# Kernel tuning notes

Hardware: AMD Instinct MI355X
Metric: run time of the kernel (lower is better)

Reference implementation:

```python
import jax, jax.numpy as jnp
import numpy as np


def _mask_finished_scores(score, flag):
    # score: (B, K); flag: (B, 1) bool. For finished rows: column 0 -> 0, columns > 0 -> -inf
    # (standard WeNet mask_finished_scores, applied both to (B, beam) and (B, V) tensors).
    K = score.shape[-1]
    col = jnp.arange(K)[None, :]
    score = jnp.where(flag & (col == 0), 0.0, score)
    return jnp.where(flag & (col > 0), -jnp.inf, score)


def _batch_beam_search(log_post, beam_size, masks):
    # log_post: (B, S, V) log-softmax; masks: (B, S) bool (True = padded/finished)
    B, S, V = log_post.shape
    eos = V - 1
    log_prob, idx0 = jax.lax.top_k(log_post[:, 0, :], beam_size)   # (B, beam)
    end_flag = masks[:, 0][:, None]                                # (B, 1)
    log_prob = _mask_finished_scores(log_prob, end_flag)
    idx0 = jnp.where(end_flag, eos, idx0)                          # mask_finished_preds

    def step(carry, xs):
        log_prob, end_flag = carry
        lp_i, m_i = xs                                             # (B, V), (B,)
        scores = _mask_finished_scores(lp_i, end_flag)             # (B, V)
        cand = log_prob[:, :, None] + scores[:, None, :]           # (B, beam, V)
        log_prob, top_idx = jax.lax.top_k(cand.reshape(B, beam_size * V), beam_size)
        idx = jnp.where(end_flag, eos, top_idx)                    # mask_finished_preds
        return (log_prob, m_i[:, None]), idx

    (log_prob, _), idx_rest = jax.lax.scan(
        step,
        (log_prob, end_flag),
        (jnp.swapaxes(log_post[:, 1:], 0, 1), jnp.swapaxes(masks[:, 1:], 0, 1)),
    )
    indices = jnp.concatenate([idx0[None], idx_rest], axis=0)      # (S, B, beam)
    indices = jnp.moveaxis(indices, 0, -1)                         # (B, beam, S)
    return jnp.mod(indices, V), log_prob                           # torch.fmod(indices, vocab)


def setup_inputs() -> dict:
    key = jax.random.key(0)
    k1, k2, k3 = jax.random.split(key, 3)
    B, S, V, BEAM = 16, 128, 32000, 4
    logit = jax.random.normal(k1, (B, S, V), dtype=jnp.float32)
    asd_scores = jax.random.uniform(k2, (BEAM, B), dtype=jnp.float32)
    tgt_lens = jax.random.randint(k3, (B,), 0, S)
    return {"logit": logit, "asd_scores": asd_scores, "tgt_lens": tgt_lens, "beam_size": BEAM}


def reference(logit, asd_scores, tgt_lens, beam_size):
    B, S, V = logit.shape
    lens = jnp.clip(tgt_lens, 2, S)
    # make_pad_mask(tgt_lens - 1): True where position is padding
    masks = jnp.arange(S)[None, :] >= (lens - 1)[:, None]          # (B, S) bool
    log_post = jax.nn.log_softmax(logit, axis=-1)                  # (B, S, V)
    # beam search runs under no_grad in torch -> stop_gradient here
    indices, _ = _batch_beam_search(jax.lax.stop_gradient(log_post), beam_size, masks)
    # gather per-step log-probs along each beam path: (B, beam, S)
    glp = jnp.take_along_axis(log_post[:, None], indices[..., None], axis=-1).squeeze(-1)
    topk_log_prob = jnp.sum(jnp.where(masks[:, None, :], 0.0, glp), axis=-1)  # (B, beam)
    nbest_log_dist = topk_log_prob.T                               # (beam, B)
    # compute_masd_loss_ver2 with normalized_score=True
    w = jax.nn.softmax(nbest_log_dist, axis=0)                     # exp(d - logsumexp(d, 0))
    asd_norm = asd_scores - jnp.mean(asd_scores, axis=0)           # (beam, B)
    masd = jnp.sum(w * asd_norm, axis=0)                           # (B,)
    return jnp.mean(masd)                                          # reduction='mean'
```

## Files before the change

### kernel.cpp

```cpp
#include <hip/hip_runtime.h>
#include <math.h>

#define NB 16
#define NS 128
#define NV 32000
#define ROWS (NB*NS)
#define CAP 1024
#define T0  3.0f

#define WS_IX_OFF  (ROWS*4*sizeof(float))
#define WS_PART_OFF (WS_IX_OFF + ROWS*4*sizeof(unsigned short))

__device__ __forceinline__ bool lexgt(float av, int ai, float bv, int bi) {
    return (av > bv) || (av == bv && ai < bi);
}

__global__ __launch_bounds__(256)
void k_rowprep(const float* __restrict__ logit,
               float* __restrict__ ws_sc,
               unsigned short* __restrict__ ws_ix)
{
    const int row  = blockIdx.x;
    const int tid  = threadIdx.x;
    const int lane = tid & 63;
    const int wv   = tid >> 6;
    const float4* __restrict__ x4 = (const float4*)(logit + (size_t)row * NV);

    __shared__ float  sM[4];
    __shared__ double sE[4];
    __shared__ int    s_cnt;
    __shared__ __align__(16) char smem[16384];
    float* s_cv = (float*)smem;
    int*   s_ci = (int*)(smem + CAP*4);
    float* stv  = (float*)smem;
    int*   sti  = (int*)(smem + 8192);

    if (tid == 0) s_cnt = 0;
    __syncthreads();

    float m = -INFINITY;
    double e0 = 0.0, e1 = 0.0, e2 = 0.0, e3 = 0.0;

#define PROC(q, base)                                                                            \
    {                                                                                            \
        float mx = fmaxf(fmaxf((q).x, (q).y), fmaxf((q).z, (q).w));                              \
        m = fmaxf(m, mx);                                                                        \
        e0 += (double)__expf((q).x);                                                             \
        e1 += (double)__expf((q).y);                                                             \
        e2 += (double)__expf((q).z);                                                             \
        e3 += (double)__expf((q).w);                                                             \
        if (mx >= T0) {                                                                          \
            if ((q).x >= T0) { int p = atomicAdd(&s_cnt, 1); if (p < CAP) { s_cv[p] = (q).x; s_ci[p] = 4*(base)+0; } } \
            if ((q).y >= T0) { int p = atomicAdd(&s_cnt, 1); if (p < CAP) { s_cv[p] = (q).y; s_ci[p] = 4*(base)+1; } } \
            if ((q).z >= T0) { int p = atomicAdd(&s_cnt, 1); if (p < CAP) { s_cv[p] = (q).z; s_ci[p] = 4*(base)+2; } } \
            if ((q).w >= T0) { int p = atomicAdd(&s_cnt, 1); if (p < CAP) { s_cv[p] = (q).w; s_ci[p] = 4*(base)+3; } } \
        }                                                                                        \
    }

#pragma unroll 1
    for (int k = 0; k < 7; ++k) {
        const int i = tid + k*1024;
        float4 q0 = x4[i];
        float4 q1 = x4[i + 256];
        float4 q2 = x4[i + 512];
        float4 q3 = x4[i + 768];
        PROC(q0, i);
        PROC(q1, i + 256);
        PROC(q2, i + 512);
        PROC(q3, i + 768);
    }
    for (int i = 7168 + tid; i < NV/4; i += 256) {
        float4 q = x4[i];
        PROC(q, i);
    }
#undef PROC

    float gm = m;
    gm = fmaxf(gm, __shfl_xor(gm, 1));
    gm = fmaxf(gm, __shfl_xor(gm, 2));
    gm = fmaxf(gm, __shfl_xor(gm, 4));
    float Tw = gm;
    Tw = fminf(Tw, __shfl_xor(Tw, 8));
    Tw = fminf(Tw, __shfl_xor(Tw, 16));
    Tw = fminf(Tw, __shfl_xor(Tw, 32));
    float wm = gm;
    wm = fmaxf(wm, __shfl_xor(wm, 8));
    wm = fmaxf(wm, __shfl_xor(wm, 16));
    wm = fmaxf(wm, __shfl_xor(wm, 32));
    double es = ((e0 + e1) + (e2 + e3));
    es += __shfl_xor(es, 1);
    es += __shfl_xor(es, 2);
    es += __shfl_xor(es, 4);
    es += __shfl_xor(es, 8);
    es += __shfl_xor(es, 16);
    es += __shfl_xor(es, 32);

    if (lane == 0) { sM[wv] = wm; sE[wv] = es; }
    __syncthreads();

    const float  M    = fmaxf(fmaxf(sM[0], sM[1]), fmaxf(sM[2], sM[3]));
    const double Esum = ((sE[0] + sE[1]) + (sE[2] + sE[3]));
    int cnt = s_cnt;

    bool fast = (cnt >= 8) && (cnt <= CAP);
    if (!fast) {
        __syncthreads();
        if (tid == 0) s_cnt = 0;
        __syncthreads();
        for (int i = tid; i < NV/4; i += 256) {
            float4 q = x4[i];
            float mx = fmaxf(fmaxf(q.x, q.y), fmaxf(q.z, q.w));
            if (mx >= Tw) {
                if (q.x >= Tw) { int p = atomicAdd(&s_cnt, 1); if (p < CAP) { s_cv[p] = q.x; s_ci[p] = 4*i+0; } }
                if (q.y >= Tw) { int p = atomicAdd(&s_cnt, 1); if (p < CAP) { s_cv[p] = q.y; s_ci[p] = 4*i+1; } }
                if (q.z >= Tw) { int p = atomicAdd(&s_cnt, 1); if (p < CAP) { s_cv[p] = q.z; s_ci[p] = 4*i+2; } }
                if (q.w >= Tw) { int p = atomicAdd(&s_cnt, 1); if (p < CAP) { s_cv[p] = q.w; s_ci[p] = 4*i+3; } }
            }
        }
        __syncthreads();
        cnt = s_cnt;
    }

    if (cnt <= CAP) {
        if (wv == 0) {
            float tv[8]; int ti[8];
#pragma unroll
            for (int j = 0; j < 8; ++j) { tv[j] = -INFINITY; ti[j] = 0x7fffffff; }
            for (int c = lane; c < cnt; c += 64) {
                float v = s_cv[c]; int gi = s_ci[c];
                if (lexgt(v, gi, tv[7], ti[7])) {
                    tv[7] = v; ti[7] = gi;
#pragma unroll
                    for (int p = 7; p > 0; --p) {
                        if (lexgt(tv[p], ti[p], tv[p-1], ti[p-1])) {
                            float fv = tv[p]; tv[p] = tv[p-1]; tv[p-1] = fv;
                            int   fi = ti[p]; ti[p] = ti[p-1]; ti[p-1] = fi;
                        }
                    }
                }
            }
            float bv[8]; int bi[8];
#pragma unroll
            for (int r = 0; r < 8; ++r) {
                float hv = tv[0]; int hi = ti[0];
#pragma unroll
                for (int d = 1; d <= 32; d <<= 1) {
                    float ov = __shfl_xor(hv, d); int oi = __shfl_xor(hi, d);
                    if (lexgt(ov, oi, hv, hi)) { hv = ov; hi = oi; }
                }
                bv[r] = hv; bi[r] = hi;
                if (ti[0] == hi) {
#pragma unroll
                    for (int p = 0; p < 7; ++p) { tv[p] = tv[p+1]; ti[p] = ti[p+1]; }
                    tv[7] = -INFINITY; ti[7] = 0x7fffffff;
                }
            }
            if (lane == 0) {
                float slse = (float)(log(Esum) - (double)M);
                float sc[8]; int ix[8];
#pragma unroll
                for (int j = 0; j < 8; ++j) { sc[j] = (bv[j] - M) - slse; ix[j] = bi[j]; }
#pragma unroll
                for (int pass = 0; pass < 8; ++pass) {
#pragma unroll
                    for (int j = 0; j < 7; ++j) {
                        if (lexgt(sc[j+1], ix[j+1], sc[j], ix[j])) {
                            float fv = sc[j]; sc[j] = sc[j+1]; sc[j+1] = fv;
                            int   fi = ix[j]; ix[j] = ix[j+1]; ix[j+1] = fi;
                        }
                    }
                }
#pragma unroll
                for (int j = 0; j < 4; ++j) {
                    ws_sc[row*4+j] = sc[j];
                    ws_ix[row*4+j] = (unsigned short)ix[j];
                }
            }
        }
    } else {
        float tv[8]; int ti[8];
#pragma unroll
        for (int j = 0; j < 8; ++j) { tv[j] = -INFINITY; ti[j] = 0x7fffffff; }
        for (int i = tid; i < NV/4; i += 256) {
            float4 q = x4[i];
#pragma unroll
            for (int c = 0; c < 4; ++c) {
                float v = (c==0)?q.x:(c==1)?q.y:(c==2)?q.z:q.w;
                int gi = 4*i + c;
                if (lexgt(v, gi, tv[7], ti[7])) {
                    tv[7] = v; ti[7] = gi;
#pragma unroll
                    for (int p = 7; p > 0; --p) {
                        if (lexgt(tv[p], ti[p], tv[p-1], ti[p-1])) {
                            float fv = tv[p]; tv[p] = tv[p-1]; tv[p-1] = fv;
                            int   fi = ti[p]; ti[p] = ti[p-1]; ti[p-1] = fi;
                        }
                    }
                }
            }
        }
        __syncthreads();
#pragma unroll
        for (int j = 0; j < 8; ++j) { stv[tid*8+j] = tv[j]; sti[tid*8+j] = ti[j]; }
        __syncthreads();
        for (int st = 128; st >= 1; st >>= 1) {
            if (tid < st) {
                int pa = 0, pb = 0;
                float ov[8]; int oi[8];
#pragma unroll
                for (int j = 0; j < 8; ++j) {
                    float av = stv[tid*8+pa];      int aix = sti[tid*8+pa];
                    float bv = stv[(tid+st)*8+pb]; int bix = sti[(tid+st)*8+pb];
                    bool ta = lexgt(av, aix, bv, bix);
                    ov[j] = ta ? av : bv;
                    oi[j] = ta ? aix : bix;
                    pa += ta ? 1 : 0;
                    pb += ta ? 0 : 1;
                }
#pragma unroll
                for (int j = 0; j < 8; ++j) { stv[tid*8+j] = ov[j]; sti[tid*8+j] = oi[j]; }
            }
            __syncthreads();
        }
        if (tid == 0) {
            float slse = (float)(log(Esum) - (double)M);
            float sc[8]; int ix[8];
#pragma unroll
            for (int j = 0; j < 8; ++j) { sc[j] = (stv[j] - M) - slse; ix[j] = sti[j]; }
#pragma unroll
            for (int pass = 0; pass < 8; ++pass) {
#pragma unroll
                for (int j = 0; j < 7; ++j) {
                    if (lexgt(sc[j+1], ix[j+1], sc[j], ix[j])) {
                        float fv = sc[j]; sc[j] = sc[j+1]; sc[j+1] = fv;
                        int   fi = ix[j]; ix[j] = ix[j+1]; ix[j+1] = fi;
                    }
                }
            }
#pragma unroll
            for (int j = 0; j < 4; ++j) {
                ws_sc[row*4+j] = sc[j];
                ws_ix[row*4+j] = (unsigned short)ix[j];
            }
        }
    }
}

__global__ __launch_bounds__(64)
void k_beam(const float* __restrict__ ws_sc,
            const unsigned short* __restrict__ ws_ix,
            const float* __restrict__ asd,
            const int*   __restrict__ tlen,
            float* __restrict__ ws_part)
{
    const int b = blockIdx.x;
    const int lane = threadIdx.x;

    __shared__ float4  Lsc[NS];
    __shared__ ushort4 Lix[NS];
    {
        const float4*  sc4p = (const float4*)ws_sc;
        const ushort4* ix4p = (const ushort4*)ws_ix;
        for (int i = lane; i < NS; i += 64) {
            Lsc[i] = sc4p[b*NS + i];
            Lix[i] = ix4p[b*NS + i];
        }
    }
    __syncthreads();

    int L = tlen[b];
    L = L < 2 ? 2 : (L > NS ? NS : L);

    const int ci = lane & 15;
    const int k  = ci >> 2;
    const int r  = ci & 3;

    float4 sc0 = Lsc[0];
    float c0 = sc0.x, c1 = sc0.y, c2 = sc0.z, c3 = sc0.w;
    double sum0 = sc0.x, sum1 = sc0.y, sum2 = sc0.z, sum3 = sc0.w;

    float4 scN = Lsc[1]; ushort4 ixN = Lix[1];

    for (int s = 1; s <= L-2; ++s) {
        float4 sc = scN; ushort4 ix = ixN;
        scN = Lsc[s+1]; ixN = Lix[s+1];

        float myscore = (r==0)?sc.x:(r==1)?sc.y:(r==2)?sc.z:sc.w;
        int   myidx   = (r==0)?ix.x:(r==1)?ix.y:(r==2)?ix.z:ix.w;
        float mycarry = (k==0)?c0:(k==1)?c1:(k==2)?c2:c3;
        float cand = mycarry + myscore;
        int   flat = k*NV + myidx;

        int g = lane >> 4;
        int rp = 0;
#pragma unroll
        for (int mm = 0; mm < 4; ++mm) {
            int j = g*4 + mm;
            float cj = __shfl(cand, j);
            int   fj = __shfl(flat, j);
            rp += ((cj > cand) || (cj == cand && fj < flat)) ? 1 : 0;
        }
        int rank = __shfl(rp, ci) + __shfl(rp, ci+16) + __shfl(rp, ci+32) + __shfl(rp, ci+48);

        float nc0, nc1, nc2, nc3, ns0, ns1, ns2, ns3;
        {
            unsigned long long m0 = __ballot(rank == 0 && lane < 16);
            int sl = __ffsll(m0) - 1;
            nc0 = __shfl(cand, sl); ns0 = __shfl(myscore, sl);
        }
        {
            unsigned long long m1 = __ballot(rank == 1 && lane < 16);
            int sl = __ffsll(m1) - 1;
            nc1 = __shfl(cand, sl); ns1 = __shfl(myscore, sl);
        }
        {
            unsigned long long m2 = __ballot(rank == 2 && lane < 16);
            int sl = __ffsll(m2) - 1;
            nc2 = __shfl(cand, sl); ns2 = __shfl(myscore, sl);
        }
        {
            unsigned long long m3 = __ballot(rank == 3 && lane < 16);
            int sl = __ffsll(m3) - 1;
            nc3 = __shfl(cand, sl); ns3 = __shfl(myscore, sl);
        }
        c0 = nc0; c1 = nc1; c2 = nc2; c3 = nc3;
        sum0 += ns0; sum1 += ns1; sum2 += ns2; sum3 += ns3;
    }

    if (lane == 0) {
        double t0 = sum0, t1 = sum1, t2 = sum2, t3 = sum3;
        double mx = fmax(fmax(t0, t1), fmax(t2, t3));
        double e0 = exp(t0 - mx), e1 = exp(t1 - mx), e2 = exp(t2 - mx), e3 = exp(t3 - mx);
        double Z = e0 + e1 + e2 + e3;
        double a0 = asd[0*16 + b], a1 = asd[1*16 + b], a2 = asd[2*16 + b], a3 = asd[3*16 + b];
        double am = (a0 + a1 + a2 + a3) * 0.25;
        double masd = (e0*(a0-am) + e1*(a1-am) + e2*(a2-am) + e3*(a3-am)) / Z;
        ws_part[b] = (float)masd;
    }
}

__global__ __launch_bounds__(64)
void k_final(const float* __restrict__ ws_part, float* __restrict__ out)
{
    if (threadIdx.x == 0) {
        double accd = 0.0;
#pragma unroll
        for (int i = 0; i < 16; ++i) accd += (double)ws_part[i];
        out[0] = (float)(accd / 16.0);
    }
}

extern "C" void kernel_launch(void* const* d_in, const int* in_sizes, int n_in,
                              void* d_out, int out_size, void* d_ws, size_t ws_size,
                              hipStream_t stream) {
    const float* logit = (const float*)d_in[0];
    const float* asd   = (const float*)d_in[1];
    const int*   tlen  = (const int*)d_in[2];
    float*          ws_sc   = (float*)d_ws;
    unsigned short* ws_ix   = (unsigned short*)((char*)d_ws + WS_IX_OFF);
    float*          ws_part = (float*)((char*)d_ws + WS_PART_OFF);

    k_rowprep<<<ROWS, 256, 0, stream>>>(logit, ws_sc, ws_ix);
    k_beam<<<NB, 64, 0, stream>>>(ws_sc, ws_ix, asd, tlen, ws_part);
    k_final<<<1, 64, 0, stream>>>(ws_part, (float*)d_out);
}
```

Measured before the change: 97.39 us.

## Prefetch row loads, permute-based beam reorder, fuse final reduction via ticket

The row-prep loop now software-pipelines its loads, issuing the next group of four float4 loads before processing the current group so that memory latency overlaps with compute. The beam kernel keeps each beam's carry in one lane and reorders beams with ds_permute/ds_bpermute, replacing four ballot/ffs/shuffle rounds per step and shortening the serial dependency chain. The separate final-reduction kernel is removed: the last beam block, chosen by an atomic ticket, sums the partial results, which saves one kernel launch. This relies on the ticket being reset at the start of row-prep and on threadfence ordering.

```diff
diff --git a/kernel.cpp b/kernel.cpp
--- a/kernel.cpp
+++ b/kernel.cpp
@@ -8,8 +8,9 @@
 #define CAP 1024
 #define T0  3.0f
 
-#define WS_IX_OFF  (ROWS*4*sizeof(float))
+#define WS_IX_OFF   (ROWS*4*sizeof(float))
 #define WS_PART_OFF (WS_IX_OFF + ROWS*4*sizeof(unsigned short))
+#define WS_TKT_OFF  (WS_PART_OFF + 16*sizeof(float))
 
 __device__ __forceinline__ bool lexgt(float av, int ai, float bv, int bi) {
     return (av > bv) || (av == bv && ai < bi);
@@ -18,13 +19,16 @@
 __global__ __launch_bounds__(256)
 void k_rowprep(const float* __restrict__ logit,
                float* __restrict__ ws_sc,
-               unsigned short* __restrict__ ws_ix)
+               unsigned short* __restrict__ ws_ix,
+               unsigned int* __restrict__ ticket)
 {
     const int row  = blockIdx.x;
     const int tid  = threadIdx.x;
     const int lane = tid & 63;
     const int wv   = tid >> 6;
     const float4* __restrict__ x4 = (const float4*)(logit + (size_t)row * NV);
+
+    if (row == 0 && tid == 0) *ticket = 0u;
 
     __shared__ float  sM[4];
     __shared__ double sE[4];
@@ -57,17 +61,27 @@
         }                                                                                        \
     }
 
+    float4 a0 = x4[tid], a1 = x4[tid + 256], a2 = x4[tid + 512], a3 = x4[tid + 768];
 #pragma unroll 1
-    for (int k = 0; k < 7; ++k) {
-        const int i = tid + k*1024;
-        float4 q0 = x4[i];
-        float4 q1 = x4[i + 256];
-        float4 q2 = x4[i + 512];
-        float4 q3 = x4[i + 768];
-        PROC(q0, i);
-        PROC(q1, i + 256);
-        PROC(q2, i + 512);
-        PROC(q3, i + 768);
+    for (int k = 0; k < 6; ++k) {
+        const int ib = tid + (k+1)*1024;
+        float4 b0 = x4[ib];
+        float4 b1 = x4[ib + 256];
+        float4 b2 = x4[ib + 512];
+        float4 b3 = x4[ib + 768];
+        const int ia = tid + k*1024;
+        PROC(a0, ia);
+        PROC(a1, ia + 256);
+        PROC(a2, ia + 512);
+        PROC(a3, ia + 768);
+        a0 = b0; a1 = b1; a2 = b2; a3 = b3;
+    }
+    {
+        const int ia = tid + 6*1024;
+        PROC(a0, ia);
+        PROC(a1, ia + 256);
+        PROC(a2, ia + 512);
+        PROC(a3, ia + 768);
     }
     for (int i = 7168 + tid; i < NV/4; i += 256) {
         float4 q = x4[i];
@@ -251,7 +265,9 @@
             const unsigned short* __restrict__ ws_ix,
             const float* __restrict__ asd,
             const int*   __restrict__ tlen,
-            float* __restrict__ ws_part)
+            float* __restrict__ ws_part,
+            unsigned int* __restrict__ ticket,
+            float* __restrict__ out)
 {
     const int b = blockIdx.x;
     const int lane = threadIdx.x;
@@ -276,8 +292,8 @@
     const int r  = ci & 3;
 
     float4 sc0 = Lsc[0];
-    float c0 = sc0.x, c1 = sc0.y, c2 = sc0.z, c3 = sc0.w;
-    double sum0 = sc0.x, sum1 = sc0.y, sum2 = sc0.z, sum3 = sc0.w;
+    float  c   = (lane==0)?sc0.x:(lane==1)?sc0.y:(lane==2)?sc0.z:sc0.w;
+    double sum = (double)c;
 
     float4 scN = Lsc[1]; ushort4 ixN = Lix[1];
 
@@ -287,7 +303,7 @@
 
         float myscore = (r==0)?sc.x:(r==1)?sc.y:(r==2)?sc.z:sc.w;
         int   myidx   = (r==0)?ix.x:(r==1)?ix.y:(r==2)?ix.z:ix.w;
-        float mycarry = (k==0)?c0:(k==1)?c1:(k==2)?c2:c3;
+        float mycarry = __int_as_float(__builtin_amdgcn_ds_bpermute(k << 2, __float_as_int(c)));
         float cand = mycarry + myscore;
         int   flat = k*NV + myidx;
 
@@ -302,33 +318,16 @@
         }
         int rank = __shfl(rp, ci) + __shfl(rp, ci+16) + __shfl(rp, ci+32) + __shfl(rp, ci+48);
 
-        float nc0, nc1, nc2, nc3, ns0, ns1, ns2, ns3;
-        {
-            unsigned long long m0 = __ballot(rank == 0 && lane < 16);
-            int sl = __ffsll(m0) - 1;
-            nc0 = __shfl(cand, sl); ns0 = __shfl(myscore, sl);
-        }
-        {
-            unsigned long long m1 = __ballot(rank == 1 && lane < 16);
-            int sl = __ffsll(m1) - 1;
-            nc1 = __shfl(cand, sl); ns1 = __shfl(myscore, sl);
-        }
-        {
-            unsigned long long m2 = __ballot(rank == 2 && lane < 16);
-            int sl = __ffsll(m2) - 1;
-            nc2 = __shfl(cand, sl); ns2 = __shfl(myscore, sl);
-        }
-        {
-            unsigned long long m3 = __ballot(rank == 3 && lane < 16);
-            int sl = __ffsll(m3) - 1;
-            nc3 = __shfl(cand, sl); ns3 = __shfl(myscore, sl);
-        }
-        c0 = nc0; c1 = nc1; c2 = nc2; c3 = nc3;
-        sum0 += ns0; sum1 += ns1; sum2 += ns2; sum3 += ns3;
-    }
+        int dst = (rank < 4) ? (rank << 2) : 252;
+        int nc_i = __builtin_amdgcn_ds_permute(dst, __float_as_int(cand));
+        int ns_i = __builtin_amdgcn_ds_permute(dst, __float_as_int(myscore));
+        c = __int_as_float(nc_i);
+        sum += (lane < 4) ? (double)__int_as_float(ns_i) : 0.0;
+    }
+
+    double t0 = __shfl(sum, 0), t1 = __shfl(sum, 1), t2 = __shfl(sum, 2), t3 = __shfl(sum, 3);
 
     if (lane == 0) {
-        double t0 = sum0, t1 = sum1, t2 = sum2, t3 = sum3;
         double mx = fmax(fmax(t0, t1), fmax(t2, t3));
         double e0 = exp(t0 - mx), e1 = exp(t1 - mx), e2 = exp(t2 - mx), e3 = exp(t3 - mx);
         double Z = e0 + e1 + e2 + e3;
@@ -336,17 +335,16 @@
         double am = (a0 + a1 + a2 + a3) * 0.25;
         double masd = (e0*(a0-am) + e1*(a1-am) + e2*(a2-am) + e3*(a3-am)) / Z;
         ws_part[b] = (float)masd;
-    }
-}
-
-__global__ __launch_bounds__(64)
-void k_final(const float* __restrict__ ws_part, float* __restrict__ out)
-{
-    if (threadIdx.x == 0) {
-        double accd = 0.0;
-#pragma unroll
-        for (int i = 0; i < 16; ++i) accd += (double)ws_part[i];
-        out[0] = (float)(accd / 16.0);
+        __threadfence();
+        unsigned int t = atomicAdd(ticket, 1u);
+        if (t == 15u) {
+            __threadfence();
+            double accd = 0.0;
+#pragma unroll
+            for (int i = 0; i < 16; ++i) accd += (double)ws_part[i];
+            out[0] = (float)(accd / 16.0);
+            *ticket = 0u;
+        }
     }
 }
 
@@ -359,8 +357,8 @@
     float*          ws_sc   = (float*)d_ws;
     unsigned short* ws_ix   = (unsigned short*)((char*)d_ws + WS_IX_OFF);
     float*          ws_part = (float*)((char*)d_ws + WS_PART_OFF);
-
-    k_rowprep<<<ROWS, 256, 0, stream>>>(logit, ws_sc, ws_ix);
-    k_beam<<<NB, 64, 0, stream>>>(ws_sc, ws_ix, asd, tlen, ws_part);
-    k_final<<<1, 64, 0, stream>>>(ws_part, (float*)d_out);
+    unsigned int*   ticket  = (unsigned int*)((char*)d_ws + WS_TKT_OFF);
+
+    k_rowprep<<<ROWS, 256, 0, stream>>>(logit, ws_sc, ws_ix, ticket);
+    k_beam<<<NB, 64, 0, stream>>>(ws_sc, ws_ix, asd, tlen, ws_part, ticket, (float*)d_out);
 }
```

Result: faster. 85.63 us (-12.1%).
